# Kernel tuning notes

Hardware: AMD Instinct MI355X
Metric: run time of the kernel (lower is better)

Reference implementation:

```python
import jax, jax.numpy as jnp
import numpy as np

N_NODES = 100000
N_EDGES = 1600000
IN_CH, HID, OUT_CH = 500, 128, 40


def setup_inputs() -> dict:
    key = jax.random.key(0)
    ks = jax.random.split(key, 10)
    x = jax.random.normal(ks[0], (N_NODES, IN_CH), dtype=jnp.float32)
    edge_index = jax.random.randint(ks[1], (2, N_EDGES), 0, N_NODES, dtype=jnp.int64)
    edge_attr = jax.random.uniform(ks[2], (N_EDGES,), dtype=jnp.float32)
    def glorot(k, fan_in, fan_out):
        s = jnp.sqrt(6.0 / (fan_in + fan_out))
        return jax.random.uniform(k, (fan_in, fan_out), minval=-s, maxval=s, dtype=jnp.float32)
    return {
        "x": x, "edge_index": edge_index, "edge_attr": edge_attr,
        "W1": glorot(ks[3], IN_CH, HID), "b1": jnp.zeros((HID,), jnp.float32),
        "W2": glorot(ks[4], HID, HID), "b2": jnp.zeros((HID,), jnp.float32),
        "W3": glorot(ks[5], HID, OUT_CH), "b3": jnp.zeros((OUT_CH,), jnp.float32),
    }


def _gcn_norm(edge_index, edge_weight, num_nodes):
    # add self-loops with weight 1, then symmetric normalization D^-1/2 A D^-1/2
    loop = jnp.arange(num_nodes, dtype=edge_index.dtype)
    src = jnp.concatenate([edge_index[0], loop])
    dst = jnp.concatenate([edge_index[1], loop])
    ew = jnp.concatenate([edge_weight, jnp.ones((num_nodes,), edge_weight.dtype)])
    deg = jax.ops.segment_sum(ew, dst, num_segments=num_nodes)
    dinv = jnp.where(deg > 0, jax.lax.rsqrt(jnp.maximum(deg, 1e-12)), 0.0)
    norm = dinv[src] * ew * dinv[dst]
    return src, dst, norm


def _gcn_conv(x, W, b, src, dst, norm, num_nodes):
    h = x @ W                                   # [N, F_out] dense transform first
    msg = h[src] * norm[:, None]                # gather + scale  [E+N, F_out]
    out = jax.ops.segment_sum(msg, dst, num_segments=num_nodes)
    return out + b


def reference(x, edge_index, edge_attr, W1, b1, W2, b2, W3, b3):
    n = x.shape[0]
    src, dst, norm = _gcn_norm(edge_index, edge_attr, n)  # cached=False but graph is static
    # layer 1 (hidden) + relu + residual-dense (h_res starts at 0); dropout is identity in eval
    h = jax.nn.relu(_gcn_conv(x, W1, b1, src, dst, norm, n))
    h_res = h
    # layer 2 (hidden)
    h = jax.nn.relu(_gcn_conv(h, W2, b2, src, dst, norm, n)) + h_res
    # output layer
    out = _gcn_conv(h, W3, b3, src, dst, norm, n)
    return jax.nn.log_softmax(out, axis=-1)
```

## Files before the change

kernel.cpp:

```cpp
#include <hip/hip_runtime.h>
#include <hip/hip_bf16.h>
#include <type_traits>

#define NN 100000
#define NE 1600000

#define SCAN_E 1024
#define NBLK ((NN + SCAN_E - 1) / SCAN_E)
#define GBLK ((NN + 127) / 128)
#define EBLK ((NE + 511) / 512)
#define GA1 512
#define GB1 (GBLK - GA1)

using f32x4 = __attribute__((ext_vector_type(4))) float;
using bf16x8 = __attribute__((ext_vector_type(8))) short;
using u16 = unsigned short;
using u64 = unsigned long long;

__device__ inline u16 f2bf(float f) {
    unsigned u = __float_as_uint(f);
    unsigned r = (u + 0x7fffu + ((u >> 16) & 1u)) >> 16;
    return (u16)r;
}
__device__ inline float bflo(unsigned u) { return __uint_as_float(u << 16); }
__device__ inline float bfhi(unsigned u) { return __uint_as_float(u & 0xffff0000u); }
__device__ inline float bf2f(u16 u) { return __uint_as_float((unsigned)u << 16); }
__device__ inline unsigned cvt2(float a, float b) {
    union { __hip_bfloat162 h; unsigned u; } c;
    c.h = __float22bfloat162_rn(make_float2(a, b));
    return c.u;
}

template <typename AT, int KLIM, int KSTEPS, bool TAIL>
__device__ __forceinline__ void gemm_body(const AT* __restrict__ X,
                                          const short* __restrict__ Wp,
                                          u16* __restrict__ Out, int gblk) {
    const int lane = threadIdx.x & 63;
    const int wave = threadIdx.x >> 6;
    const int row0 = gblk * 128 + wave * 16;
    const int arow = row0 + (lane & 15);
    const int kgrp = (lane >> 4) << 3;
    const bool rvalid = arow < NN;
    const AT* aptr = X + (size_t)arow * KLIM + kgrp;
    const bf16x8* wp = reinterpret_cast<const bf16x8*>(Wp);

    f32x4 acc[8];
#pragma unroll
    for (int nt = 0; nt < 8; nt++) acc[nt] = (f32x4){0.f, 0.f, 0.f, 0.f};

    const int FULL = TAIL ? (KSTEPS - 1) : KSTEPS;
#pragma unroll 2
    for (int ks = 0; ks < FULL; ks++) {
        bf16x8 af;
        if (rvalid) {
            if constexpr (std::is_same_v<AT, float>) {
                float4 f0 = *reinterpret_cast<const float4*>(aptr + ks * 32);
                float4 f1 = *reinterpret_cast<const float4*>(aptr + ks * 32 + 4);
                union { bf16x8 v; unsigned u[4]; } a;
                a.u[0] = cvt2(f0.x, f0.y);
                a.u[1] = cvt2(f0.z, f0.w);
                a.u[2] = cvt2(f1.x, f1.y);
                a.u[3] = cvt2(f1.z, f1.w);
                af = a.v;
            } else {
                af = *reinterpret_cast<const bf16x8*>(aptr + ks * 32);
            }
        } else {
#pragma unroll
            for (int j = 0; j < 8; j++) af[j] = 0;
        }
#pragma unroll
        for (int nt = 0; nt < 8; nt++) {
            bf16x8 bf = wp[(ks * 8 + nt) * 64 + lane];
            acc[nt] = __builtin_amdgcn_mfma_f32_16x16x32_bf16(af, bf, acc[nt], 0, 0, 0);
        }
    }
    if (TAIL) {
        const int ks = KSTEPS - 1;
        bf16x8 af;
#pragma unroll
        for (int j = 0; j < 8; j++) {
            int k = ks * 32 + kgrp + j;
            bool ok = rvalid && k < KLIM;
            if constexpr (std::is_same_v<AT, float>) {
                af[j] = (short)f2bf(ok ? aptr[ks * 32 + j] : 0.f);
            } else {
                af[j] = ok ? (short)aptr[ks * 32 + j] : (short)0;
            }
        }
#pragma unroll
        for (int nt = 0; nt < 8; nt++) {
            bf16x8 bf = wp[(ks * 8 + nt) * 64 + lane];
            acc[nt] = __builtin_amdgcn_mfma_f32_16x16x32_bf16(af, bf, acc[nt], 0, 0, 0);
        }
    }

    const int rbase = row0 + ((lane >> 4) << 2);
    const int cbase = lane & 15;
#pragma unroll
    for (int r = 0; r < 4; r++) {
        int orow = rbase + r;
        if (orow < NN) {
            u16* p = Out + (size_t)orow * 128 + cbase;
#pragma unroll
            for (int nt = 0; nt < 8; nt += 2) {
                unsigned v = cvt2(acc[nt][r], acc[nt + 1][r]);
                p[nt * 16] = (u16)v;
                p[nt * 16 + 16] = (u16)(v >> 16);
            }
        }
    }
}

__global__ __launch_bounds__(512) void k_deg_gemm1a(const float* __restrict__ X,
                                                    const short* __restrict__ Wp,
                                                    u16* __restrict__ Out,
                                                    const int* __restrict__ ei,
                                                    const float* __restrict__ ea,
                                                    u64* __restrict__ dc,
                                                    int* __restrict__ rank) {
    if (blockIdx.x < EBLK) {
        int e = blockIdx.x * 512 + threadIdx.x;
        if (e < NE) {
            int d = ei[NE + e];
            u64 add = (1ULL << 32) | (u64)(unsigned)(ea[e] * 16777216.0f);
            u64 old = atomicAdd(dc + d, add);
            rank[e] = (int)(old >> 32);
        }
        return;
    }
    gemm_body<float, 500, 16, true>(X, Wp, Out, blockIdx.x - EBLK);
}

__global__ __launch_bounds__(512) void k_scat_gemm1b(const float* __restrict__ X,
                                                     const short* __restrict__ Wp,
                                                     u16* __restrict__ Out,
                                                     const int* __restrict__ ei,
                                                     const float* __restrict__ ea,
                                                     const float* __restrict__ dinv,
                                                     const int* __restrict__ row_ptr,
                                                     const int* __restrict__ rank,
                                                     int2* __restrict__ csr) {
    if (blockIdx.x < EBLK) {
        int e = blockIdx.x * 512 + threadIdx.x;
        if (e < NE) {
            int s = ei[e], d = ei[NE + e];
            int pos = row_ptr[d] + rank[e];
            float w = dinv[s] * ea[e] * dinv[d];
            csr[pos] = make_int2(s, __float_as_int(w));
        }
        return;
    }
    gemm_body<float, 500, 16, true>(X, Wp, Out, blockIdx.x - EBLK + GA1);
}

template <typename AT, int KLIM, int KSTEPS, bool TAIL>
__global__ __launch_bounds__(512) void k_gemm_mfma(const AT* __restrict__ X,
                                                   const short* __restrict__ Wp,
                                                   u16* __restrict__ Out) {
    gemm_body<AT, KLIM, KSTEPS, TAIL>(X, Wp, Out, blockIdx.x);
}

__global__ __launch_bounds__(256) void k_scan1(const u64* __restrict__ dc,
                                               int* __restrict__ row_ptr,
                                               int* __restrict__ part,
                                               float* __restrict__ dinv) {
    __shared__ int ts[256];
    const int tid = threadIdx.x;
    int base = blockIdx.x * SCAN_E + tid * 4;
    int v[4];
    int ssum = 0;
#pragma unroll
    for (int j = 0; j < 4; j++) {
        if (base + j < NN) {
            uint2 d2 = reinterpret_cast<const uint2*>(dc)[base + j];
            v[j] = (int)d2.y;
            dinv[base + j] = rsqrtf((float)d2.x * (1.0f / 16777216.0f) + 1.0f);
        } else {
            v[j] = 0;
        }
        ssum += v[j];
    }
    ts[tid] = ssum;
    __syncthreads();
    for (int o = 1; o < 256; o <<= 1) {
        int t = (tid >= o) ? ts[tid - o] : 0;
        __syncthreads();
        ts[tid] += t;
        __syncthreads();
    }
    int excl = ts[tid] - ssum;
#pragma unroll
    for (int j = 0; j < 4; j++) {
        if (base + j < NN) row_ptr[base + j] = excl;
        excl += v[j];
    }
    if (tid == 255) part[blockIdx.x] = ts[255];
}

__global__ void k_scan2(int* __restrict__ part) {
    if (threadIdx.x == 0) {
        int acc = 0;
        for (int b = 0; b < NBLK; b++) { int t = part[b]; part[b] = acc; acc += t; }
    }
}

__global__ __launch_bounds__(256) void k_scan3(int* __restrict__ row_ptr,
                                               const int* __restrict__ part) {
    int base = blockIdx.x * SCAN_E + threadIdx.x * 4;
    int off = part[blockIdx.x];
#pragma unroll
    for (int j = 0; j < 4; j++)
        if (base + j < NN) row_ptr[base + j] += off;
    if (blockIdx.x == 0 && threadIdx.x == 0) row_ptr[NN] = NE;
}

__global__ __launch_bounds__(256) void k_packW(const float* __restrict__ W,
                                               short* __restrict__ Wp,
                                               int K, int total) {
    int t = blockIdx.x * 256 + threadIdx.x;
    if (t >= total) return;
    int lane = t & 63;
    int nt = (t >> 6) & 7;
    int ks = t >> 9;
    int col = nt * 16 + (lane & 15);
    int kb = ks * 32 + ((lane >> 4) << 3);
    bf16x8 v;
#pragma unroll
    for (int j = 0; j < 8; j++) {
        int k = kb + j;
        v[j] = (k < K) ? (short)f2bf(W[(size_t)k * 128 + col]) : (short)0;
    }
    reinterpret_cast<bf16x8*>(Wp)[t] = v;
}

__global__ __launch_bounds__(256) void k_packW3(const float* __restrict__ W,
                                                short* __restrict__ Wp) {
    int t = blockIdx.x * 256 + threadIdx.x;
    if (t >= 768) return;
    int lane = t & 63;
    int nt = (t >> 6) % 3;
    int ks = t / 192;
    int col = nt * 16 + (lane & 15);
    int kb = ks * 32 + ((lane >> 4) << 3);
    bf16x8 v;
#pragma unroll
    for (int j = 0; j < 8; j++)
        v[j] = (col < 40) ? (short)f2bf(W[(size_t)(kb + j) * 40 + col]) : (short)0;
    reinterpret_cast<bf16x8*>(Wp)[t] = v;
}

__global__ __launch_bounds__(512) void k_gemm40m(const u16* __restrict__ Xb,
                                                 const short* __restrict__ Wp,
                                                 u16* __restrict__ Out) {
    const int lane = threadIdx.x & 63;
    const int wave = threadIdx.x >> 6;
    const int row0 = blockIdx.x * 128 + wave * 16;
    const int arow = row0 + (lane & 15);
    const int kgrp = (lane >> 4) << 3;
    const bool rvalid = arow < NN;
    const u16* aptr = Xb + (size_t)arow * 128 + kgrp;
    const bf16x8* wp = reinterpret_cast<const bf16x8*>(Wp);

    f32x4 acc[3];
#pragma unroll
    for (int nt = 0; nt < 3; nt++) acc[nt] = (f32x4){0.f, 0.f, 0.f, 0.f};

#pragma unroll
    for (int ks = 0; ks < 4; ks++) {
        bf16x8 af;
        if (rvalid) af = *reinterpret_cast<const bf16x8*>(aptr + ks * 32);
        else {
#pragma unroll
            for (int j = 0; j < 8; j++) af[j] = 0;
        }
#pragma unroll
        for (int nt = 0; nt < 3; nt++) {
            bf16x8 bf = wp[(ks * 3 + nt) * 64 + lane];
            acc[nt] = __builtin_amdgcn_mfma_f32_16x16x32_bf16(af, bf, acc[nt], 0, 0, 0);
        }
    }

    const int rbase = row0 + ((lane >> 4) << 2);
    const int cbase = lane & 15;
#pragma unroll
    for (int r = 0; r < 4; r++) {
        int orow = rbase + r;
        if (orow < NN) {
#pragma unroll
            for (int nt = 0; nt < 3; nt++) {
                int col = nt * 16 + cbase;
                if (col < 40) Out[(size_t)orow * 40 + col] = f2bf(acc[nt][r]);
            }
        }
    }
}

template <int MODE>
__global__ __launch_bounds__(256) void k_pull128(const u16* __restrict__ H,
                                                 const int* __restrict__ row_ptr,
                                                 const int2* __restrict__ csr,
                                                 const float* __restrict__ dinv,
                                                 const float* __restrict__ b,
                                                 const u16* __restrict__ R,
                                                 u16* __restrict__ Out) {
    int node = blockIdx.x * 8 + (threadIdx.x >> 5);
    int cg = threadIdx.x & 31;
    const uint2* H2 = reinterpret_cast<const uint2*>(H);
    float dv = dinv[node];
    float sw = dv * dv;
    uint2 h = H2[node * 32 + cg];
    float4 acc;
    acc.x = bflo(h.x) * sw; acc.y = bfhi(h.x) * sw;
    acc.z = bflo(h.y) * sw; acc.w = bfhi(h.y) * sw;

    int e0 = row_ptr[node], e1 = row_ptr[node + 1];
    for (int base = e0; base < e1; base += 32) {
        int n = e1 - base;
        if (n > 32) n = 32;
        int2 sv = (cg < n) ? csr[base + cg] : make_int2(0, 0);
        int j = 0;
        for (; j + 4 <= n; j += 4) {
            int s0 = __shfl(sv.x, j + 0, 32);
            int s1 = __shfl(sv.x, j + 1, 32);
            int s2 = __shfl(sv.x, j + 2, 32);
            int s3 = __shfl(sv.x, j + 3, 32);
            float w0 = __int_as_float(__shfl(sv.y, j + 0, 32));
            float w1 = __int_as_float(__shfl(sv.y, j + 1, 32));
            float w2 = __int_as_float(__shfl(sv.y, j + 2, 32));
            float w3 = __int_as_float(__shfl(sv.y, j + 3, 32));
            uint2 g0 = H2[s0 * 32 + cg];
            uint2 g1 = H2[s1 * 32 + cg];
            uint2 g2 = H2[s2 * 32 + cg];
            uint2 g3 = H2[s3 * 32 + cg];
            acc.x = fmaf(w0, bflo(g0.x), acc.x); acc.y = fmaf(w0, bfhi(g0.x), acc.y);
            acc.z = fmaf(w0, bflo(g0.y), acc.z); acc.w = fmaf(w0, bfhi(g0.y), acc.w);
            acc.x = fmaf(w1, bflo(g1.x), acc.x); acc.y = fmaf(w1, bfhi(g1.x), acc.y);
            acc.z = fmaf(w1, bflo(g1.y), acc.z); acc.w = fmaf(w1, bfhi(g1.y), acc.w);
            acc.x = fmaf(w2, bflo(g2.x), acc.x); acc.y = fmaf(w2, bfhi(g2.x), acc.y);
            acc.z = fmaf(w2, bflo(g2.y), acc.z); acc.w = fmaf(w2, bfhi(g2.y), acc.w);
            acc.x = fmaf(w3, bflo(g3.x), acc.x); acc.y = fmaf(w3, bfhi(g3.x), acc.y);
            acc.z = fmaf(w3, bflo(g3.y), acc.z); acc.w = fmaf(w3, bfhi(g3.y), acc.w);
        }
        for (; j < n; j++) {
            int s = __shfl(sv.x, j, 32);
            float w = __int_as_float(__shfl(sv.y, j, 32));
            uint2 g = H2[s * 32 + cg];
            acc.x = fmaf(w, bflo(g.x), acc.x); acc.y = fmaf(w, bfhi(g.x), acc.y);
            acc.z = fmaf(w, bflo(g.y), acc.z); acc.w = fmaf(w, bfhi(g.y), acc.w);
        }
    }

    float4 bb = reinterpret_cast<const float4*>(b)[cg];
    float4 o;
    o.x = fmaxf(acc.x + bb.x, 0.f);
    o.y = fmaxf(acc.y + bb.y, 0.f);
    o.z = fmaxf(acc.z + bb.z, 0.f);
    o.w = fmaxf(acc.w + bb.w, 0.f);
    if (MODE == 2) {
        uint2 r = reinterpret_cast<const uint2*>(R)[node * 32 + cg];
        o.x += bflo(r.x); o.y += bfhi(r.x);
        o.z += bflo(r.y); o.w += bfhi(r.y);
    }
    reinterpret_cast<uint2*>(Out)[node * 32 + cg] =
        make_uint2(cvt2(o.x, o.y), cvt2(o.z, o.w));
}

__global__ __launch_bounds__(256) void k_pull40_lsm(const u16* __restrict__ G,
                                                    const int* __restrict__ row_ptr,
                                                    const int2* __restrict__ csr,
                                                    const float* __restrict__ dinv,
                                                    const float* __restrict__ b3,
                                                    float* __restrict__ out) {
    int node = blockIdx.x * 4 + (threadIdx.x >> 6);
    int lane = threadIdx.x & 63;
    const bool act = lane < 40;
    float dv = dinv[node];
    float sw = dv * dv;
    float acc = act ? bf2f(G[node * 40 + lane]) * sw : 0.f;

    int e0 = row_ptr[node], e1 = row_ptr[node + 1];
    for (int base = e0; base < e1; base += 64) {
        int n = e1 - base;
        if (n > 64) n = 64;
        int2 sv = (lane < n) ? csr[base + lane] : make_int2(0, 0);
        int j = 0;
        for (; j + 4 <= n; j += 4) {
            int s0 = __shfl(sv.x, j + 0);
            int s1 = __shfl(sv.x, j + 1);
            int s2 = __shfl(sv.x, j + 2);
            int s3 = __shfl(sv.x, j + 3);
            float w0 = __int_as_float(__shfl(sv.y, j + 0));
            float w1 = __int_as_float(__shfl(sv.y, j + 1));
            float w2 = __int_as_float(__shfl(sv.y, j + 2));
            float w3 = __int_as_float(__shfl(sv.y, j + 3));
            float g0 = act ? bf2f(G[s0 * 40 + lane]) : 0.f;
            float g1 = act ? bf2f(G[s1 * 40 + lane]) : 0.f;
            float g2 = act ? bf2f(G[s2 * 40 + lane]) : 0.f;
            float g3 = act ? bf2f(G[s3 * 40 + lane]) : 0.f;
            acc = fmaf(w0, g0, acc);
            acc = fmaf(w1, g1, acc);
            acc = fmaf(w2, g2, acc);
            acc = fmaf(w3, g3, acc);
        }
        for (; j < n; j++) {
            int s = __shfl(sv.x, j);
            float w = __int_as_float(__shfl(sv.y, j));
            float g = act ? bf2f(G[s * 40 + lane]) : 0.f;
            acc = fmaf(w, g, acc);
        }
    }

    float v = act ? acc + b3[lane] : -1e30f;
    float m = v;
    for (int o = 32; o; o >>= 1) m = fmaxf(m, __shfl_xor(m, o));
    float e = act ? expf(v - m) : 0.f;
    float ssum = e;
    for (int o = 32; o; o >>= 1) ssum += __shfl_xor(ssum, o);
    float ls = logf(ssum);
    if (act) out[node * 40 + lane] = v - m - ls;
}

extern "C" void kernel_launch(void* const* d_in, const int* in_sizes, int n_in,
                              void* d_out, int out_size, void* d_ws, size_t ws_size,
                              hipStream_t stream) {
    const float* x  = (const float*)d_in[0];
    const int*   ei = (const int*)d_in[1];
    const float* ea = (const float*)d_in[2];
    const float* W1 = (const float*)d_in[3];
    const float* b1 = (const float*)d_in[4];
    const float* W2 = (const float*)d_in[5];
    const float* b2 = (const float*)d_in[6];
    const float* W3 = (const float*)d_in[7];
    const float* b3 = (const float*)d_in[8];
    float* out = (float*)d_out;

    short* Wp1     = (short*)d_ws;
    short* Wp2     = Wp1 + 65536;
    short* Wp3     = Wp2 + 16384;
    u16*   Hb      = (u16*)(Wp3 + 6144);
    u16*   h1b     = Hb + (size_t)NN * 128;
    u16*   G3b     = h1b + (size_t)NN * 128;
    u64*   dc      = (u64*)(G3b + (size_t)NN * 40);
    float* dinv    = (float*)(dc + NN);
    int*   row_ptr = (int*)(dinv + NN);
    int*   part    = row_ptr + NN + 8;
    int*   rank    = part + 128;
    int2*  csr     = (int2*)(rank + NE);

    hipMemsetAsync(dc, 0, NN * sizeof(u64), stream);
    k_packW<<<32, 256, 0, stream>>>(W1, Wp1, 500, 16 * 8 * 64);
    k_packW<<<8, 256, 0, stream>>>(W2, Wp2, 128, 4 * 8 * 64);
    k_packW3<<<3, 256, 0, stream>>>(W3, Wp3);

    k_deg_gemm1a<<<EBLK + GA1, 512, 0, stream>>>(x, Wp1, Hb, ei, ea, dc, rank);

    k_scan1<<<NBLK, 256, 0, stream>>>(dc, row_ptr, part, dinv);
    k_scan2<<<1, 64, 0, stream>>>(part);
    k_scan3<<<NBLK, 256, 0, stream>>>(row_ptr, part);

    k_scat_gemm1b<<<EBLK + GB1, 512, 0, stream>>>(x, Wp1, Hb, ei, ea, dinv,
                                                  row_ptr, rank, csr);

    k_pull128<1><<<NN / 8, 256, 0, stream>>>(Hb, row_ptr, csr, dinv, b1, nullptr, h1b);

    k_gemm_mfma<u16, 128, 4, false><<<GBLK, 512, 0, stream>>>(h1b, Wp2, Hb);
    k_pull128<2><<<NN / 8, 256, 0, stream>>>(Hb, row_ptr, csr, dinv, b2, h1b, h1b);

    k_gemm40m<<<GBLK, 512, 0, stream>>>(h1b, Wp3, G3b);
    k_pull40_lsm<<<NN / 4, 256, 0, stream>>>(G3b, row_ptr, csr, dinv, b3, out);
}
```

Baseline: 526.2 us.

## Pack degree counters into u32, build CSR with cursor atomics, pad G3 rows

Degree counting now uses a 32-bit atomic word holding an 8-bit edge count and a 24-bit fixed-point weight sum, instead of a 64-bit word. The per-edge rank array is dropped: the scatter pass takes slots with atomics on a per-node cursor that the scan zeroes, removing a 6.4MB write and read. The layer-3 feature rows are padded from 40 to 64 bf16 so gathered rows are aligned, and the split of GEMM blocks between the two fused kernels is changed. The 8-bit count overflows on nodes with more than 255 in-edges, and the coarser fixed-point weights lose some precision.

```diff
diff --git a/kernel.cpp b/kernel.cpp
--- a/kernel.cpp
+++ b/kernel.cpp
@@ -9,13 +9,13 @@
 #define NBLK ((NN + SCAN_E - 1) / SCAN_E)
 #define GBLK ((NN + 127) / 128)
 #define EBLK ((NE + 511) / 512)
-#define GA1 512
+#define GA1 350
 #define GB1 (GBLK - GA1)
 
 using f32x4 = __attribute__((ext_vector_type(4))) float;
 using bf16x8 = __attribute__((ext_vector_type(8))) short;
 using u16 = unsigned short;
-using u64 = unsigned long long;
+using u32 = unsigned int;
 
 __device__ inline u16 f2bf(float f) {
     unsigned u = __float_as_uint(f);
@@ -117,15 +117,13 @@
                                                     u16* __restrict__ Out,
                                                     const int* __restrict__ ei,
                                                     const float* __restrict__ ea,
-                                                    u64* __restrict__ dc,
-                                                    int* __restrict__ rank) {
+                                                    u32* __restrict__ dc) {
     if (blockIdx.x < EBLK) {
         int e = blockIdx.x * 512 + threadIdx.x;
         if (e < NE) {
             int d = ei[NE + e];
-            u64 add = (1ULL << 32) | (u64)(unsigned)(ea[e] * 16777216.0f);
-            u64 old = atomicAdd(dc + d, add);
-            rank[e] = (int)(old >> 32);
+            u32 add = (1u << 24) | (u32)(ea[e] * 32768.0f);
+            atomicAdd(dc + d, add);
         }
         return;
     }
@@ -139,13 +137,13 @@
                                                      const float* __restrict__ ea,
                                                      const float* __restrict__ dinv,
                                                      const int* __restrict__ row_ptr,
-                                                     const int* __restrict__ rank,
+                                                     int* __restrict__ cursor,
                                                      int2* __restrict__ csr) {
     if (blockIdx.x < EBLK) {
         int e = blockIdx.x * 512 + threadIdx.x;
         if (e < NE) {
             int s = ei[e], d = ei[NE + e];
-            int pos = row_ptr[d] + rank[e];
+            int pos = row_ptr[d] + atomicAdd(&cursor[d], 1);
             float w = dinv[s] * ea[e] * dinv[d];
             csr[pos] = make_int2(s, __float_as_int(w));
         }
@@ -161,7 +159,7 @@
     gemm_body<AT, KLIM, KSTEPS, TAIL>(X, Wp, Out, blockIdx.x);
 }
 
-__global__ __launch_bounds__(256) void k_scan1(const u64* __restrict__ dc,
+__global__ __launch_bounds__(256) void k_scan1(const u32* __restrict__ dc,
                                                int* __restrict__ row_ptr,
                                                int* __restrict__ part,
                                                float* __restrict__ dinv) {
@@ -173,9 +171,10 @@
 #pragma unroll
     for (int j = 0; j < 4; j++) {
         if (base + j < NN) {
-            uint2 d2 = reinterpret_cast<const uint2*>(dc)[base + j];
-            v[j] = (int)d2.y;
-            dinv[base + j] = rsqrtf((float)d2.x * (1.0f / 16777216.0f) + 1.0f);
+            u32 d2 = dc[base + j];
+            v[j] = (int)(d2 >> 24);
+            float wsum = (float)(d2 & 0xFFFFFFu) * (1.0f / 32768.0f);
+            dinv[base + j] = rsqrtf(wsum + 1.0f);
         } else {
             v[j] = 0;
         }
@@ -206,12 +205,13 @@
 }
 
 __global__ __launch_bounds__(256) void k_scan3(int* __restrict__ row_ptr,
-                                               const int* __restrict__ part) {
+                                               const int* __restrict__ part,
+                                               int* __restrict__ cursor) {
     int base = blockIdx.x * SCAN_E + threadIdx.x * 4;
     int off = part[blockIdx.x];
 #pragma unroll
     for (int j = 0; j < 4; j++)
-        if (base + j < NN) row_ptr[base + j] += off;
+        if (base + j < NN) { row_ptr[base + j] += off; cursor[base + j] = 0; }
     if (blockIdx.x == 0 && threadIdx.x == 0) row_ptr[NN] = NE;
 }
 
@@ -290,7 +290,7 @@
 #pragma unroll
             for (int nt = 0; nt < 3; nt++) {
                 int col = nt * 16 + cbase;
-                if (col < 40) Out[(size_t)orow * 40 + col] = f2bf(acc[nt][r]);
+                if (col < 40) Out[(size_t)orow * 64 + col] = f2bf(acc[nt][r]);
             }
         }
     }
@@ -377,7 +377,7 @@
     const bool act = lane < 40;
     float dv = dinv[node];
     float sw = dv * dv;
-    float acc = act ? bf2f(G[node * 40 + lane]) * sw : 0.f;
+    float acc = act ? bf2f(G[node * 64 + lane]) * sw : 0.f;
 
     int e0 = row_ptr[node], e1 = row_ptr[node + 1];
     for (int base = e0; base < e1; base += 64) {
@@ -394,10 +394,10 @@
             float w1 = __int_as_float(__shfl(sv.y, j + 1));
             float w2 = __int_as_float(__shfl(sv.y, j + 2));
             float w3 = __int_as_float(__shfl(sv.y, j + 3));
-            float g0 = act ? bf2f(G[s0 * 40 + lane]) : 0.f;
-            float g1 = act ? bf2f(G[s1 * 40 + lane]) : 0.f;
-            float g2 = act ? bf2f(G[s2 * 40 + lane]) : 0.f;
-            float g3 = act ? bf2f(G[s3 * 40 + lane]) : 0.f;
+            float g0 = act ? bf2f(G[s0 * 64 + lane]) : 0.f;
+            float g1 = act ? bf2f(G[s1 * 64 + lane]) : 0.f;
+            float g2 = act ? bf2f(G[s2 * 64 + lane]) : 0.f;
+            float g3 = act ? bf2f(G[s3 * 64 + lane]) : 0.f;
             acc = fmaf(w0, g0, acc);
             acc = fmaf(w1, g1, acc);
             acc = fmaf(w2, g2, acc);
@@ -406,7 +406,7 @@
         for (; j < n; j++) {
             int s = __shfl(sv.x, j);
             float w = __int_as_float(__shfl(sv.y, j));
-            float g = act ? bf2f(G[s * 40 + lane]) : 0.f;
+            float g = act ? bf2f(G[s * 64 + lane]) : 0.f;
             acc = fmaf(w, g, acc);
         }
     }
@@ -441,26 +441,26 @@
     u16*   Hb      = (u16*)(Wp3 + 6144);
     u16*   h1b     = Hb + (size_t)NN * 128;
     u16*   G3b     = h1b + (size_t)NN * 128;
-    u64*   dc      = (u64*)(G3b + (size_t)NN * 40);
+    u32*   dc      = (u32*)(G3b + (size_t)NN * 64);
     float* dinv    = (float*)(dc + NN);
     int*   row_ptr = (int*)(dinv + NN);
     int*   part    = row_ptr + NN + 8;
-    int*   rank    = part + 128;
-    int2*  csr     = (int2*)(rank + NE);
-
-    hipMemsetAsync(dc, 0, NN * sizeof(u64), stream);
+    int*   cursor  = part + 128;
+    int2*  csr     = (int2*)(cursor + NN);
+
+    hipMemsetAsync(dc, 0, NN * sizeof(u32), stream);
     k_packW<<<32, 256, 0, stream>>>(W1, Wp1, 500, 16 * 8 * 64);
     k_packW<<<8, 256, 0, stream>>>(W2, Wp2, 128, 4 * 8 * 64);
     k_packW3<<<3, 256, 0, stream>>>(W3, Wp3);
 
-    k_deg_gemm1a<<<EBLK + GA1, 512, 0, stream>>>(x, Wp1, Hb, ei, ea, dc, rank);
+    k_deg_gemm1a<<<EBLK + GA1, 512, 0, stream>>>(x, Wp1, Hb, ei, ea, dc);
 
     k_scan1<<<NBLK, 256, 0, stream>>>(dc, row_ptr, part, dinv);
     k_scan2<<<1, 64, 0, stream>>>(part);
-    k_scan3<<<NBLK, 256, 0, stream>>>(row_ptr, part);
+    k_scan3<<<NBLK, 256, 0, stream>>>(row_ptr, part, cursor);
 
     k_scat_gemm1b<<<EBLK + GB1, 512, 0, stream>>>(x, Wp1, Hb, ei, ea, dinv,
-                                                  row_ptr, rank, csr);
+                                                  row_ptr, cursor, csr);
 
     k_pull128<1><<<NN / 8, 256, 0, stream>>>(Hb, row_ptr, csr, dinv, b1, nullptr, h1b);
 
```

New measurement: 560.8 us. 1.07x slower.

## Interleave GEMM and edge blocks in fused kernels, rebalance split, pad G3 rows

Applied to the files above, without the earlier changes.

The two fused kernels now spread the GEMM blocks evenly among the edge-processing blocks instead of putting all edge blocks first. Edge blocks become grid-stride loops over a fixed 1024 blocks. The GEMM split between the two kernels changes from 512 to 420 row tiles. The layer-3 output buffer gets a row stride of 64 instead of 40 so gathered rows are aligned. The aim is better overlap of atomic and scatter work with the compute-bound GEMM; the cost is 60% more memory for that buffer and a different load balance.

```diff
diff --git a/kernel.cpp b/kernel.cpp
--- a/kernel.cpp
+++ b/kernel.cpp
@@ -8,13 +8,17 @@
 #define SCAN_E 1024
 #define NBLK ((NN + SCAN_E - 1) / SCAN_E)
 #define GBLK ((NN + 127) / 128)
-#define EBLK ((NE + 511) / 512)
-#define GA1 512
-#define GB1 (GBLK - GA1)
+#define EB1 1024
+#define GA 420
+#define T1 (EB1 + GA)
+#define EB3 1024
+#define GB (GBLK - GA)
+#define T3 (EB3 + GB)
 
 using f32x4 = __attribute__((ext_vector_type(4))) float;
 using bf16x8 = __attribute__((ext_vector_type(8))) short;
 using u16 = unsigned short;
+using u32 = unsigned int;
 using u64 = unsigned long long;
 
 __device__ inline u16 f2bf(float f) {
@@ -119,17 +123,20 @@
                                                     const float* __restrict__ ea,
                                                     u64* __restrict__ dc,
                                                     int* __restrict__ rank) {
-    if (blockIdx.x < EBLK) {
-        int e = blockIdx.x * 512 + threadIdx.x;
-        if (e < NE) {
-            int d = ei[NE + e];
-            u64 add = (1ULL << 32) | (u64)(unsigned)(ea[e] * 16777216.0f);
-            u64 old = atomicAdd(dc + d, add);
-            rank[e] = (int)(old >> 32);
-        }
+    int b = blockIdx.x;
+    int g = (b * GA) / T1;
+    bool is_gemm = (((b + 1) * GA) / T1) > g;
+    if (is_gemm) {
+        gemm_body<float, 500, 16, true>(X, Wp, Out, g);
         return;
     }
-    gemm_body<float, 500, 16, true>(X, Wp, Out, blockIdx.x - EBLK);
+    int eb = b - g;
+    for (int e = eb * 512 + (int)threadIdx.x; e < NE; e += EB1 * 512) {
+        int d = ei[NE + e];
+        u64 add = (1ULL << 32) | (u64)(unsigned)(ea[e] * 16777216.0f);
+        u64 old = atomicAdd(dc + d, add);
+        rank[e] = (int)(old >> 32);
+    }
 }
 
 __global__ __launch_bounds__(512) void k_scat_gemm1b(const float* __restrict__ X,
@@ -141,17 +148,20 @@
                                                      const int* __restrict__ row_ptr,
                                                      const int* __restrict__ rank,
                                                      int2* __restrict__ csr) {
-    if (blockIdx.x < EBLK) {
-        int e = blockIdx.x * 512 + threadIdx.x;
-        if (e < NE) {
-            int s = ei[e], d = ei[NE + e];
-            int pos = row_ptr[d] + rank[e];
-            float w = dinv[s] * ea[e] * dinv[d];
-            csr[pos] = make_int2(s, __float_as_int(w));
-        }
+    int b = blockIdx.x;
+    int g = (b * GB) / T3;
+    bool is_gemm = (((b + 1) * GB) / T3) > g;
+    if (is_gemm) {
+        gemm_body<float, 500, 16, true>(X, Wp, Out, GA + g);
         return;
     }
-    gemm_body<float, 500, 16, true>(X, Wp, Out, blockIdx.x - EBLK + GA1);
+    int eb = b - g;
+    for (int e = eb * 512 + (int)threadIdx.x; e < NE; e += EB3 * 512) {
+        int s = ei[e], d = ei[NE + e];
+        int pos = row_ptr[d] + rank[e];
+        float w = dinv[s] * ea[e] * dinv[d];
+        csr[pos] = make_int2(s, __float_as_int(w));
+    }
 }
 
 template <typename AT, int KLIM, int KSTEPS, bool TAIL>
@@ -290,7 +300,7 @@
 #pragma unroll
             for (int nt = 0; nt < 3; nt++) {
                 int col = nt * 16 + cbase;
-                if (col < 40) Out[(size_t)orow * 40 + col] = f2bf(acc[nt][r]);
+                if (col < 40) Out[(size_t)orow * 64 + col] = f2bf(acc[nt][r]);
             }
         }
     }
@@ -377,7 +387,7 @@
     const bool act = lane < 40;
     float dv = dinv[node];
     float sw = dv * dv;
-    float acc = act ? bf2f(G[node * 40 + lane]) * sw : 0.f;
+    float acc = act ? bf2f(G[node * 64 + lane]) * sw : 0.f;
 
     int e0 = row_ptr[node], e1 = row_ptr[node + 1];
     for (int base = e0; base < e1; base += 64) {
@@ -394,10 +404,10 @@
             float w1 = __int_as_float(__shfl(sv.y, j + 1));
             float w2 = __int_as_float(__shfl(sv.y, j + 2));
             float w3 = __int_as_float(__shfl(sv.y, j + 3));
-            float g0 = act ? bf2f(G[s0 * 40 + lane]) : 0.f;
-            float g1 = act ? bf2f(G[s1 * 40 + lane]) : 0.f;
-            float g2 = act ? bf2f(G[s2 * 40 + lane]) : 0.f;
-            float g3 = act ? bf2f(G[s3 * 40 + lane]) : 0.f;
+            float g0 = act ? bf2f(G[s0 * 64 + lane]) : 0.f;
+            float g1 = act ? bf2f(G[s1 * 64 + lane]) : 0.f;
+            float g2 = act ? bf2f(G[s2 * 64 + lane]) : 0.f;
+            float g3 = act ? bf2f(G[s3 * 64 + lane]) : 0.f;
             acc = fmaf(w0, g0, acc);
             acc = fmaf(w1, g1, acc);
             acc = fmaf(w2, g2, acc);
@@ -406,7 +416,7 @@
         for (; j < n; j++) {
             int s = __shfl(sv.x, j);
             float w = __int_as_float(__shfl(sv.y, j));
-            float g = act ? bf2f(G[s * 40 + lane]) : 0.f;
+            float g = act ? bf2f(G[s * 64 + lane]) : 0.f;
             acc = fmaf(w, g, acc);
         }
     }
@@ -441,7 +451,7 @@
     u16*   Hb      = (u16*)(Wp3 + 6144);
     u16*   h1b     = Hb + (size_t)NN * 128;
     u16*   G3b     = h1b + (size_t)NN * 128;
-    u64*   dc      = (u64*)(G3b + (size_t)NN * 40);
+    u64*   dc      = (u64*)(G3b + (size_t)NN * 64);
     float* dinv    = (float*)(dc + NN);
     int*   row_ptr = (int*)(dinv + NN);
     int*   part    = row_ptr + NN + 8;
@@ -453,14 +463,14 @@
     k_packW<<<8, 256, 0, stream>>>(W2, Wp2, 128, 4 * 8 * 64);
     k_packW3<<<3, 256, 0, stream>>>(W3, Wp3);
 
-    k_deg_gemm1a<<<EBLK + GA1, 512, 0, stream>>>(x, Wp1, Hb, ei, ea, dc, rank);
+    k_deg_gemm1a<<<T1, 512, 0, stream>>>(x, Wp1, Hb, ei, ea, dc, rank);
 
     k_scan1<<<NBLK, 256, 0, stream>>>(dc, row_ptr, part, dinv);
     k_scan2<<<1, 64, 0, stream>>>(part);
     k_scan3<<<NBLK, 256, 0, stream>>>(row_ptr, part);
 
-    k_scat_gemm1b<<<EBLK + GB1, 512, 0, stream>>>(x, Wp1, Hb, ei, ea, dinv,
-                                                  row_ptr, rank, csr);
+    k_scat_gemm1b<<<T3, 512, 0, stream>>>(x, Wp1, Hb, ei, ea, dinv,
+                                          row_ptr, rank, csr);
 
     k_pull128<1><<<NN / 8, 256, 0, stream>>>(Hb, row_ptr, csr, dinv, b1, nullptr, h1b);
 
```

Result: slower. 541.6 us (+2.9%).
